# Kernel tuning notes

Hardware: AMD Instinct MI355X
Metric: run time of the kernel (lower is better)

Reference implementation:

```python
import jax, jax.numpy as jnp
import numpy as np

EMBED = 1024
HEADS = 16
HEAD_DIM = EMBED // HEADS


def setup_inputs() -> dict:
    key = jax.random.key(0)
    k1, k2, k3 = jax.random.split(key, 3)
    hidden_states = jax.random.normal(k1, (2, 2048, EMBED), dtype=jnp.float32)
    # Conv1D weights are stored (nx, nf): y = x @ W + b
    c_attn_w = jax.random.normal(k2, (EMBED, 3 * EMBED), dtype=jnp.float32) * 0.02
    c_attn_b = jnp.zeros((3 * EMBED,), dtype=jnp.float32)
    c_proj_w = jax.random.normal(k3, (EMBED, EMBED), dtype=jnp.float32) * 0.02
    c_proj_b = jnp.zeros((EMBED,), dtype=jnp.float32)
    return {
        "hidden_states": hidden_states,
        "c_attn_w": c_attn_w,
        "c_attn_b": c_attn_b,
        "c_proj_w": c_proj_w,
        "c_proj_b": c_proj_b,
    }


def reference(hidden_states, c_attn_w, c_attn_b, c_proj_w, c_proj_b):
    B, S, E = hidden_states.shape
    H, D = HEADS, HEAD_DIM
    fused = hidden_states @ c_attn_w + c_attn_b  # [B,S,3E]
    q, k, v = jnp.split(fused, 3, axis=-1)
    # split heads -> [B,H,S,D]
    q = q.reshape(B, S, H, D).transpose(0, 2, 1, 3)
    k = k.reshape(B, S, H, D).transpose(0, 2, 1, 3)
    v = v.reshape(B, S, H, D).transpose(0, 2, 1, 3)
    scores = jnp.einsum("bhqd,bhkd->bhqk", q, k) / jnp.sqrt(jnp.float32(D))
    probs = jax.nn.softmax(scores, axis=-1)  # NOTE: no causal mask in source
    attn = jnp.einsum("bhqk,bhkd->bhqd", probs, v)
    out = attn.transpose(0, 2, 1, 3).reshape(B, S, E)
    return out @ c_proj_w + c_proj_b
```

## Files before the change

kernel.cpp:

```cpp
#include <hip/hip_runtime.h>
#include <hip/hip_bf16.h>
#include <cstdint>
#include <cstddef>

#define E_ 1024
#define H_ 16
#define D_ 64
#define B_ 2
#define S_ 2048
#define T_ 4096
#define NQ_ 3072

typedef __bf16 bf16_t;
typedef bf16_t bf16x8 __attribute__((ext_vector_type(8)));
typedef float f32x4 __attribute__((ext_vector_type(4)));

static __device__ __forceinline__ unsigned short f2bf(float f) {
    __hip_bfloat16 h = __float2bfloat16(f);
    return __builtin_bit_cast(unsigned short, h);
}
static __device__ __forceinline__ unsigned pack2(float a, float b) {
    return (unsigned)f2bf(a) | ((unsigned)f2bf(b) << 16);
}
static __device__ __forceinline__ bf16x8 ld_frag(const unsigned short* p) {
    uint4 u = *reinterpret_cast<const uint4*>(p);
    return __builtin_bit_cast(bf16x8, u);
}
static __device__ __forceinline__ void cp16(unsigned short* lds, const unsigned short* g) {
    __builtin_amdgcn_global_load_lds(
        (const __attribute__((address_space(1))) unsigned int*)g,
        (__attribute__((address_space(3))) unsigned int*)lds, 16, 0, 0);
}
static __device__ __forceinline__ f32x4 mfma16(bf16x8 a, bf16x8 b, f32x4 c) {
    return __builtin_amdgcn_mfma_f32_16x16x32_bf16(a, b, c, 0, 0, 0);
}

__global__ __launch_bounds__(256) void k_cvt(const float* __restrict__ in,
                                             unsigned short* __restrict__ out, int n) {
    int i = (blockIdx.x * 256 + threadIdx.x) * 4;
    if (i < n) {
        float4 v = *reinterpret_cast<const float4*>(in + i);
        uint2 o;
        o.x = pack2(v.x, v.y);
        o.y = pack2(v.z, v.w);
        *reinterpret_cast<uint2*>(out + i) = o;
    }
}

__global__ __launch_bounds__(256) void k_wt(const float* __restrict__ in,
                                            unsigned short* __restrict__ out, int K, int N) {
    __shared__ float t[32][33];
    int n0 = blockIdx.x * 32, k0 = blockIdx.y * 32;
    int tx = threadIdx.x, ty = threadIdx.y;
    for (int j = 0; j < 4; j++) {
        int r = ty + j * 8;
        t[r][tx] = in[(size_t)(k0 + r) * N + n0 + tx];
    }
    __syncthreads();
    for (int j = 0; j < 4; j++) {
        int r = ty + j * 8;
        out[(size_t)(n0 + r) * K + k0 + tx] = f2bf(t[tx][r]);
    }
}

static __device__ __forceinline__ void gemm_tile_128(
    const unsigned short* __restrict__ A,
    const unsigned short* __restrict__ Bt,
    int Ktot, int m0, int n0,
    unsigned short* As, unsigned short* Bs,
    f32x4 acc[4][4])
{
    const int t = threadIdx.x;
    const int w = t >> 6, lane = t & 63, lr = lane & 15, lq = lane >> 4;
    const int wm = (w >> 1) * 64, wn = (w & 1) * 64;
    for (int mt = 0; mt < 4; mt++)
        for (int nt = 0; nt < 4; nt++)
            acc[mt][nt] = (f32x4){0.f, 0.f, 0.f, 0.f};

    for (int kt = 0; kt < Ktot; kt += 32) {
        __syncthreads();
        for (int i = 0; i < 2; i++) {
            int c = t + i * 256;
            int row = c >> 2, kp = (c & 3) * 8;
            cp16(&As[c * 8], &A[(size_t)(m0 + row) * Ktot + kt + kp]);
        }
        for (int i = 0; i < 2; i++) {
            int c = t + i * 256;
            int row = c >> 2, kp = (c & 3) * 8;
            cp16(&Bs[c * 8], &Bt[(size_t)(n0 + row) * Ktot + kt + kp]);
        }
        __syncthreads();
        bf16x8 af[4], bfr[4];
        for (int mt = 0; mt < 4; mt++) af[mt]  = ld_frag(&As[(wm + mt * 16 + lr) * 32 + lq * 8]);
        for (int nt = 0; nt < 4; nt++) bfr[nt] = ld_frag(&Bs[(wn + nt * 16 + lr) * 32 + lq * 8]);
        for (int mt = 0; mt < 4; mt++)
            for (int nt = 0; nt < 4; nt++)
                acc[mt][nt] = mfma16(af[mt], bfr[nt], acc[mt][nt]);
    }
}

__global__ __launch_bounds__(256) void k_qkv(
    const unsigned short* __restrict__ Ab, const unsigned short* __restrict__ Wt,
    const float* __restrict__ bias,
    unsigned short* __restrict__ Qb, unsigned short* __restrict__ Kb,
    unsigned short* __restrict__ Vb)
{
    __shared__ __attribute__((aligned(16))) unsigned short As[128 * 32];
    __shared__ __attribute__((aligned(16))) unsigned short Bs[128 * 32];
    f32x4 acc[4][4];
    int m0 = blockIdx.x * 128, n0 = blockIdx.y * 128;
    gemm_tile_128(Ab, Wt, E_, m0, n0, As, Bs, acc);

    int t = threadIdx.x, w = t >> 6, lane = t & 63, lr = lane & 15, lq = lane >> 4;
    int wm = (w >> 1) * 64, wn = (w & 1) * 64;
    int sector = (n0 >> 10);
    for (int nt = 0; nt < 4; nt++) {
        int n = n0 + wn + nt * 16 + lr;
        float bv = bias[n];
        int nn = n & 1023, h = nn >> 6, d = nn & 63;
        for (int mt = 0; mt < 4; mt++) {
            for (int i = 0; i < 4; i++) {
                int tok = m0 + wm + mt * 16 + lq * 4 + i;
                int b = tok >> 11, s = tok & 2047;
                float v = acc[mt][nt][i] + bv;
                if (sector == 0) {
                    Qb[(((size_t)(b * H_ + h) * S_ + s) << 6) + d] = f2bf(v * 0.125f);
                } else if (sector == 1) {
                    Kb[(((size_t)(b * H_ + h) * S_ + s) << 6) + d] = f2bf(v);
                } else {
                    Vb[(((size_t)(b * H_ + h) * D_ + d) << 11) + s] = f2bf(v);
                }
            }
        }
    }
}

__global__ __launch_bounds__(256) void k_attn(
    const unsigned short* __restrict__ Qb, const unsigned short* __restrict__ Kb,
    const unsigned short* __restrict__ Vb, unsigned short* __restrict__ Ob)
{
    __shared__ __attribute__((aligned(16))) unsigned short Ks[128 * 64];
    __shared__ __attribute__((aligned(16))) unsigned short Vt[64 * 128];
    __shared__ __attribute__((aligned(16))) unsigned short Ps[4][16 * 128];

    const int t = threadIdx.x, w = t >> 6, lane = t & 63, lr = lane & 15, lq = lane >> 4;
    const int h = blockIdx.y, b = blockIdx.z;
    const size_t head = ((size_t)(b * H_ + h)) * (S_ * D_);
    const unsigned short* Qh = Qb + head;
    const unsigned short* Kh = Kb + head;
    const unsigned short* Vh = Vb + head;
    const int q0 = blockIdx.x * 64 + w * 16;
    const int swz = lr & 7;

    bf16x8 qa[2];
    for (int kk = 0; kk < 2; kk++)
        qa[kk] = ld_frag(&Qh[(size_t)(q0 + lr) * 64 + kk * 32 + lq * 8]);

    f32x4 o[4];
    for (int i = 0; i < 4; i++) o[i] = (f32x4){0.f, 0.f, 0.f, 0.f};
    float lsum = 0.f;
    unsigned short* Pw = Ps[w];

    for (int kt = 0; kt < S_; kt += 128) {
        __syncthreads();
        for (int i = 0; i < 4; i++) {
            int c = t + i * 256;
            int row = c >> 3, sp = c & 7, seg = sp ^ (row & 7);
            cp16(&Ks[c * 8], &Kh[(size_t)(kt + row) * 64 + seg * 8]);
        }
        for (int i = 0; i < 4; i++) {
            int c = t + i * 256;
            int d = c >> 4, sp = c & 15, seg = (sp & 8) | ((sp & 7) ^ (d & 7));
            cp16(&Vt[c * 8], &Vh[(size_t)d * S_ + kt + seg * 8]);
        }
        __syncthreads();

        float pexp[8][4];
        for (int tau = 0; tau < 8; tau++) {
            f32x4 z = (f32x4){0.f, 0.f, 0.f, 0.f};
            bf16x8 kf0 = ld_frag(&Ks[(tau * 16 + lr) * 64 + ((0 + lq) ^ swz) * 8]);
            bf16x8 kf1 = ld_frag(&Ks[(tau * 16 + lr) * 64 + ((4 + lq) ^ swz) * 8]);
            z = mfma16(kf0, qa[0], z);
            z = mfma16(kf1, qa[1], z);
            for (int r = 0; r < 4; r++) {
                float p = __expf(z[r]);
                pexp[tau][r] = p;
                lsum += p;
            }
        }
        for (int tau = 0; tau < 8; tau++) {
            uint2 pk;
            pk.x = pack2(pexp[tau][0], pexp[tau][1]);
            pk.y = pack2(pexp[tau][2], pexp[tau][3]);
            int seg = (tau * 2 + (lq >> 1)) ^ swz;
            *reinterpret_cast<uint2*>(&Pw[lr * 128 + seg * 8 + (lq & 1) * 4]) = pk;
        }
        for (int kk = 0; kk < 4; kk++) {
            bf16x8 pf = ld_frag(&Pw[lr * 128 + ((kk * 4 + lq) ^ swz) * 8]);
            for (int t2 = 0; t2 < 4; t2++) {
                int seg = kk * 4 + lq;
                int sp = (seg & 8) | ((seg & 7) ^ swz);
                bf16x8 vf = ld_frag(&Vt[(t2 * 16 + lr) * 128 + sp * 8]);
                o[t2] = mfma16(vf, pf, o[t2]);
            }
        }
    }

    lsum += __shfl_xor(lsum, 16, 64);
    lsum += __shfl_xor(lsum, 32, 64);
    float inv = 1.0f / lsum;

    int s = q0 + lr;
    size_t rowoff = ((size_t)(b * S_ + s)) * E_ + h * 64;
    for (int t2 = 0; t2 < 4; t2++) {
        uint2 pk;
        pk.x = pack2(o[t2][0] * inv, o[t2][1] * inv);
        pk.y = pack2(o[t2][2] * inv, o[t2][3] * inv);
        *reinterpret_cast<uint2*>(&Ob[rowoff + t2 * 16 + lq * 4]) = pk;
    }
}

__global__ __launch_bounds__(256) void k_proj(
    const unsigned short* __restrict__ Ab, const unsigned short* __restrict__ Wt,
    const float* __restrict__ bias, float* __restrict__ out)
{
    __shared__ __attribute__((aligned(16))) unsigned short As[128 * 32];
    __shared__ __attribute__((aligned(16))) unsigned short Bs[128 * 32];
    f32x4 acc[4][4];
    int m0 = blockIdx.x * 128, n0 = blockIdx.y * 128;
    gemm_tile_128(Ab, Wt, E_, m0, n0, As, Bs, acc);

    int t = threadIdx.x, w = t >> 6, lane = t & 63, lr = lane & 15, lq = lane >> 4;
    int wm = (w >> 1) * 64, wn = (w & 1) * 64;
    for (int nt = 0; nt < 4; nt++) {
        int n = n0 + wn + nt * 16 + lr;
        float bv = bias[n];
        for (int mt = 0; mt < 4; mt++)
            for (int i = 0; i < 4; i++) {
                int tok = m0 + wm + mt * 16 + lq * 4 + i;
                out[(size_t)tok * E_ + n] = acc[mt][nt][i] + bv;
            }
    }
}

extern "C" void kernel_launch(void* const* d_in, const int* in_sizes, int n_in,
                              void* d_out, int out_size, void* d_ws, size_t ws_size,
                              hipStream_t stream) {
    const float* hs = (const float*)d_in[0];
    const float* w1 = (const float*)d_in[1];
    const float* b1 = (const float*)d_in[2];
    const float* w2 = (const float*)d_in[3];
    const float* b2 = (const float*)d_in[4];
    float* out = (float*)d_out;

    char* ws = (char*)d_ws;
    unsigned short* hb  = (unsigned short*)(ws);
    unsigned short* w1t = (unsigned short*)(ws + (size_t)( 8 << 20));
    unsigned short* w2t = (unsigned short*)(ws + (size_t)(14 << 20));
    unsigned short* Qb  = (unsigned short*)(ws + (size_t)(16 << 20));
    unsigned short* Kb  = (unsigned short*)(ws + (size_t)(24 << 20));
    unsigned short* Vb  = (unsigned short*)(ws + (size_t)(32 << 20));
    unsigned short* Ao  = (unsigned short*)(ws + (size_t)(40 << 20));

    k_cvt<<<dim3(T_ * E_ / 1024), dim3(256), 0, stream>>>(hs, hb, T_ * E_);
    k_wt<<<dim3(NQ_ / 32, E_ / 32), dim3(32, 8), 0, stream>>>(w1, w1t, E_, NQ_);
    k_wt<<<dim3(E_ / 32, E_ / 32), dim3(32, 8), 0, stream>>>(w2, w2t, E_, E_);
    k_qkv<<<dim3(T_ / 128, NQ_ / 128), dim3(256), 0, stream>>>(hb, w1t, b1, Qb, Kb, Vb);
    k_attn<<<dim3(S_ / 64, H_, B_), dim3(256), 0, stream>>>(Qb, Kb, Vb, Ao);
    k_proj<<<dim3(T_ / 128, E_ / 128), dim3(256), 0, stream>>>(Ao, w2t, b2, out);
}
```

Measured before the change: 217.4 us.

## Double-buffer K/V tiles in attention and fold log2e into Q scale

The attention kernel now stages K and V through two 64-key shared-memory buffers. The next tile is loaded asynchronously while the current one is computed, which removes one of the two barriers per iteration and hides global load latency. The Q scale is changed to include log2(e) so the softmax can use the hardware exp2 instead of expf. MFMA sections are also wrapped in s_setprio. Halving the tile doubles the loop iteration count, and the exp2 change shifts rounding slightly.

Result: faster. 203.6 us (-6.4%).

```diff
diff --git a/kernel.cpp b/kernel.cpp
--- a/kernel.cpp
+++ b/kernel.cpp
@@ -124,7 +124,7 @@
                 int b = tok >> 11, s = tok & 2047;
                 float v = acc[mt][nt][i] + bv;
                 if (sector == 0) {
-                    Qb[(((size_t)(b * H_ + h) * S_ + s) << 6) + d] = f2bf(v * 0.125f);
+                    Qb[(((size_t)(b * H_ + h) * S_ + s) << 6) + d] = f2bf(v * 0.18033688f);
                 } else if (sector == 1) {
                     Kb[(((size_t)(b * H_ + h) * S_ + s) << 6) + d] = f2bf(v);
                 } else {
@@ -139,9 +139,9 @@
     const unsigned short* __restrict__ Qb, const unsigned short* __restrict__ Kb,
     const unsigned short* __restrict__ Vb, unsigned short* __restrict__ Ob)
 {
-    __shared__ __attribute__((aligned(16))) unsigned short Ks[128 * 64];
-    __shared__ __attribute__((aligned(16))) unsigned short Vt[64 * 128];
-    __shared__ __attribute__((aligned(16))) unsigned short Ps[4][16 * 128];
+    __shared__ __attribute__((aligned(16))) unsigned short Ks[2][64 * 64];
+    __shared__ __attribute__((aligned(16))) unsigned short Vt[2][64 * 64];
+    __shared__ __attribute__((aligned(16))) unsigned short Ps[4][16 * 64];
 
     const int t = threadIdx.x, w = t >> 6, lane = t & 63, lr = lane & 15, lq = lane >> 4;
     const int h = blockIdx.y, b = blockIdx.z;
@@ -161,49 +161,65 @@
     float lsum = 0.f;
     unsigned short* Pw = Ps[w];
 
-    for (int kt = 0; kt < S_; kt += 128) {
-        __syncthreads();
-        for (int i = 0; i < 4; i++) {
+    auto stage = [&](int bb, int kt) {
+        for (int i = 0; i < 2; i++) {
             int c = t + i * 256;
             int row = c >> 3, sp = c & 7, seg = sp ^ (row & 7);
-            cp16(&Ks[c * 8], &Kh[(size_t)(kt + row) * 64 + seg * 8]);
-        }
-        for (int i = 0; i < 4; i++) {
-            int c = t + i * 256;
-            int d = c >> 4, sp = c & 15, seg = (sp & 8) | ((sp & 7) ^ (d & 7));
-            cp16(&Vt[c * 8], &Vh[(size_t)d * S_ + kt + seg * 8]);
-        }
-        __syncthreads();
-
-        float pexp[8][4];
-        for (int tau = 0; tau < 8; tau++) {
+            cp16(&Ks[bb][c * 8], &Kh[(size_t)(kt + row) * 64 + seg * 8]);
+        }
+        for (int i = 0; i < 2; i++) {
+            int c = t + i * 256;
+            int d = c >> 3, sp = c & 7, seg = sp ^ (d & 7);
+            cp16(&Vt[bb][c * 8], &Vh[(size_t)d * S_ + kt + seg * 8]);
+        }
+    };
+
+    stage(0, 0);
+    asm volatile("s_waitcnt vmcnt(0)" ::: "memory");
+    __syncthreads();
+
+    int cur = 0;
+    for (int kt = 0; kt < S_; kt += 64) {
+        if (kt + 64 < S_) stage(cur ^ 1, kt + 64);
+
+        const unsigned short* Kc = Ks[cur];
+        const unsigned short* Vc = Vt[cur];
+
+        float pexp[4][4];
+        for (int tau = 0; tau < 4; tau++) {
             f32x4 z = (f32x4){0.f, 0.f, 0.f, 0.f};
-            bf16x8 kf0 = ld_frag(&Ks[(tau * 16 + lr) * 64 + ((0 + lq) ^ swz) * 8]);
-            bf16x8 kf1 = ld_frag(&Ks[(tau * 16 + lr) * 64 + ((4 + lq) ^ swz) * 8]);
+            bf16x8 kf0 = ld_frag(&Kc[(tau * 16 + lr) * 64 + ((0 + lq) ^ swz) * 8]);
+            bf16x8 kf1 = ld_frag(&Kc[(tau * 16 + lr) * 64 + ((4 + lq) ^ swz) * 8]);
+            __builtin_amdgcn_s_setprio(1);
             z = mfma16(kf0, qa[0], z);
             z = mfma16(kf1, qa[1], z);
+            __builtin_amdgcn_s_setprio(0);
             for (int r = 0; r < 4; r++) {
-                float p = __expf(z[r]);
+                float p = __builtin_amdgcn_exp2f(z[r]);
                 pexp[tau][r] = p;
                 lsum += p;
             }
         }
-        for (int tau = 0; tau < 8; tau++) {
+        for (int tau = 0; tau < 4; tau++) {
             uint2 pk;
             pk.x = pack2(pexp[tau][0], pexp[tau][1]);
             pk.y = pack2(pexp[tau][2], pexp[tau][3]);
             int seg = (tau * 2 + (lq >> 1)) ^ swz;
-            *reinterpret_cast<uint2*>(&Pw[lr * 128 + seg * 8 + (lq & 1) * 4]) = pk;
-        }
-        for (int kk = 0; kk < 4; kk++) {
-            bf16x8 pf = ld_frag(&Pw[lr * 128 + ((kk * 4 + lq) ^ swz) * 8]);
+            *reinterpret_cast<uint2*>(&Pw[lr * 64 + seg * 8 + (lq & 1) * 4]) = pk;
+        }
+        for (int kk = 0; kk < 2; kk++) {
+            bf16x8 pf = ld_frag(&Pw[lr * 64 + ((kk * 4 + lq) ^ swz) * 8]);
+            __builtin_amdgcn_s_setprio(1);
             for (int t2 = 0; t2 < 4; t2++) {
-                int seg = kk * 4 + lq;
-                int sp = (seg & 8) | ((seg & 7) ^ swz);
-                bf16x8 vf = ld_frag(&Vt[(t2 * 16 + lr) * 128 + sp * 8]);
+                bf16x8 vf = ld_frag(&Vc[(t2 * 16 + lr) * 64 + ((kk * 4 + lq) ^ swz) * 8]);
                 o[t2] = mfma16(vf, pf, o[t2]);
             }
-        }
+            __builtin_amdgcn_s_setprio(0);
+        }
+
+        asm volatile("s_waitcnt vmcnt(0)" ::: "memory");
+        __syncthreads();
+        cur ^= 1;
     }
 
     lsum += __shfl_xor(lsum, 16, 64);
```
